# Kernel tuning notes

Hardware: AMD Instinct MI355X
Metric: run time of the kernel (lower is better)

## Reference

```python
import jax, jax.numpy as jnp
import numpy as np

NV, NC, E = 100000, 50000, 800000   # var nodes, config nodes, edges per direction
K = 100                              # configs per graph (uniform -> static dense batch)
B = NC // K                          # number of graphs
DV, DC, DH, DO = 64, 16, 128, 64     # var feat, config feat, hidden, out


def _w(key, i, o):
    # kaiming_normal_ init as in _init_weights
    return jax.random.normal(key, (i, o), jnp.float32) * np.float32(np.sqrt(2.0 / i))


def setup_inputs() -> dict:
    key = jax.random.key(0)
    ks = jax.random.split(key, 16)
    return {
        "x_var": jax.random.normal(ks[0], (NV, DV), jnp.float32),
        "x_config": jax.random.normal(ks[1], (NC, DC), jnp.float32),
        "src_v2c": jax.random.randint(ks[2], (E,), 0, NV, jnp.int32),
        "dst_v2c": jax.random.randint(ks[3], (E,), 0, NC, jnp.int32),
        "src_c2v": jax.random.randint(ks[4], (E,), 0, NC, jnp.int32),
        "dst_c2v": jax.random.randint(ks[5], (E,), 0, NV, jnp.int32),
        "batch_config": jnp.arange(NC, dtype=jnp.int32) // K,
        # layer 1 SAGEConv params per edge type (lin_l has bias, lin_r has none)
        "Wl1_v2c": _w(ks[6], DV, DH), "bl1_v2c": jnp.zeros((DH,), jnp.float32), "Wr1_v2c": _w(ks[7], DC, DH),
        "Wl1_c2v": _w(ks[8], DC, DH), "bl1_c2v": jnp.zeros((DH,), jnp.float32), "Wr1_c2v": _w(ks[9], DV, DH),
        # layer 2 (output layer, jk=None -> maps to out_channels)
        "Wl2_v2c": _w(ks[10], DH, DO), "bl2_v2c": jnp.zeros((DO,), jnp.float32), "Wr2_v2c": _w(ks[11], DH, DO),
    }


def _sage(x_src, x_dst, src, dst, Wl, bl, Wr, n_dst):
    # PyG SAGEConv: lin_l(mean_{j in N(i)} x_src[j]) + lin_r(x_dst[i])
    msum = jax.ops.segment_sum(x_src[src], dst, num_segments=n_dst)            # [n_dst, d_src]
    cnt = jax.ops.segment_sum(jnp.ones(src.shape, x_src.dtype), dst, num_segments=n_dst)
    mean = msum / jnp.maximum(cnt, 1.0)[:, None]
    return mean @ Wl + bl + x_dst @ Wr


def reference(x_var, x_config, src_v2c, dst_v2c, src_c2v, dst_c2v, batch_config,
              Wl1_v2c, bl1_v2c, Wr1_v2c, Wl1_c2v, bl1_c2v, Wr1_c2v,
              Wl2_v2c, bl2_v2c, Wr2_v2c):
    # --- layer 1 (to_hetero: each node type updated by its incoming edge type), ReLU between layers ---
    h_config = jax.nn.relu(_sage(x_var, x_config, src_v2c, dst_v2c, Wl1_v2c, bl1_v2c, Wr1_v2c, NC))
    h_var = jax.nn.relu(_sage(x_config, x_var, src_c2v, dst_c2v, Wl1_c2v, bl1_c2v, Wr1_c2v, NV))
    # --- layer 2: only the 'config' output is consumed downstream ---
    o_config = _sage(h_var, h_config, src_v2c, dst_v2c, Wl2_v2c, bl2_v2c, Wr2_v2c, NC)  # [NC, DO]
    # --- to_dense_batch(x['config'], batch) -> [B, K, DO]; squeeze() is a no-op (no size-1 dims) ---
    cnt = jax.ops.segment_sum(jnp.ones((NC,), jnp.int32), batch_config, num_segments=B)
    starts = jnp.cumsum(cnt) - cnt
    pos = jnp.arange(NC, dtype=jnp.int32) - starts[batch_config]
    dense = jnp.zeros((B, K, DO), o_config.dtype).at[batch_config, pos].set(o_config)
    return dense
```

## Files before the change

kernel.cpp:

```cpp
#include <hip/hip_runtime.h>


#define CHUNK 4096
#define EPT 16
#define MAXBINS 1024

__global__ __launch_bounds__(256) void part_count2_kernel(
    const int* __restrict__ dstC, const int* __restrict__ dstV, int E, int nblocks,
    int nbinsC, int nbinsV, int* __restrict__ countsC, int* __restrict__ countsV) {
    const int* dst; int shift, nbins; int* counts; int b;
    if (blockIdx.x < (unsigned)nblocks) { dst = dstC; shift = 6; nbins = nbinsC; counts = countsC; b = blockIdx.x; }
    else { dst = dstV; shift = 7; nbins = nbinsV; counts = countsV; b = blockIdx.x - nblocks; }
    __shared__ int hist[MAXBINS];
    int t = threadIdx.x;
    for (int j = t; j < nbins; j += 256) hist[j] = 0;
    __syncthreads();
    int base = b * CHUNK;
#pragma unroll
    for (int j = 0; j < EPT; ++j) {
        int e = base + j * 256 + t;
        if (e < E) atomicAdd(&hist[dst[e] >> shift], 1);
    }
    __syncthreads();
    for (int j = t; j < nbins; j += 256) counts[(size_t)j * nblocks + b] = hist[j];
}

__global__ __launch_bounds__(256) void part_rowscan2_kernel(
    int* __restrict__ countsC, int nbinsC, int* __restrict__ binTotC,
    int* __restrict__ countsV, int* __restrict__ binTotV, int nblocks) {
    int* counts; int* binTot; int bin;
    if (blockIdx.x < (unsigned)nbinsC) { counts = countsC; binTot = binTotC; bin = blockIdx.x; }
    else { counts = countsV; binTot = binTotV; bin = blockIdx.x - nbinsC; }
    __shared__ int s[256];
    int t = threadIdx.x;
    int v = (t < nblocks) ? counts[(size_t)bin * nblocks + t] : 0;
    s[t] = v; __syncthreads();
    for (int o = 1; o < 256; o <<= 1) {
        int add = (t >= o) ? s[t - o] : 0; __syncthreads();
        s[t] += add; __syncthreads();
    }
    if (t < nblocks) counts[(size_t)bin * nblocks + t] = s[t] - v;
    if (t == nblocks - 1) binTot[bin] = s[t];
}

__global__ __launch_bounds__(256) void part_binscan2_kernel(
    const int* __restrict__ binTotC, int nbinsC, int* __restrict__ binBaseC,
    const int* __restrict__ binTotV, int nbinsV, int* __restrict__ binBaseV) {
    const int* binTot; int nbins; int* binBase;
    if (blockIdx.x == 0) { binTot = binTotC; nbins = nbinsC; binBase = binBaseC; }
    else { binTot = binTotV; nbins = nbinsV; binBase = binBaseV; }
    __shared__ int s[256];
    __shared__ int carry;
    int t = threadIdx.x;
    if (t == 0) carry = 0;
    __syncthreads();
    for (int c0 = 0; c0 < nbins; c0 += 256) {
        int v = (c0 + t < nbins) ? binTot[c0 + t] : 0;
        s[t] = v; __syncthreads();
        for (int o = 1; o < 256; o <<= 1) {
            int add = (t >= o) ? s[t - o] : 0; __syncthreads();
            s[t] += add; __syncthreads();
        }
        if (c0 + t < nbins) binBase[c0 + t] = carry + s[t] - v;
        __syncthreads();
        if (t == 255) carry += s[255];
        __syncthreads();
    }
    if (t == 0) binBase[nbins] = carry;
}

__global__ __launch_bounds__(256) void part_scatter2_kernel(
    const int* __restrict__ srcC, const int* __restrict__ dstC,
    const int* __restrict__ srcV, const int* __restrict__ dstV, int E, int nblocks,
    int nbinsC, const int* __restrict__ countsC, const int* __restrict__ binBaseC,
    int* __restrict__ ebufC,
    int nbinsV, const int* __restrict__ countsV, const int* __restrict__ binBaseV,
    int* __restrict__ ebufV) {
    const int *src, *dst, *counts, *binBase; int* ebuf; int shift, mask, nbins; int b;
    if (blockIdx.x < (unsigned)nblocks) {
        src = srcC; dst = dstC; counts = countsC; binBase = binBaseC; ebuf = ebufC;
        shift = 6; mask = 63; nbins = nbinsC; b = blockIdx.x;
    } else {
        src = srcV; dst = dstV; counts = countsV; binBase = binBaseV; ebuf = ebufV;
        shift = 7; mask = 127; nbins = nbinsV; b = blockIdx.x - nblocks;
    }
    __shared__ int hist[MAXBINS];
    int t = threadIdx.x;
    for (int j = t; j < nbins; j += 256) hist[j] = 0;
    __syncthreads();
    int base = b * CHUNK;
#pragma unroll
    for (int j = 0; j < EPT; ++j) {
        int e = base + j * 256 + t;
        if (e < E) {
            int d = dst[e];
            int bin = d >> shift;
            int rank = atomicAdd(&hist[bin], 1);
            int slot = binBase[bin] + counts[(size_t)bin * nblocks + b] + rank;
            ebuf[slot] = (src[e] << shift) | (d & mask);
        }
    }
}

__global__ __launch_bounds__(256) void csr2_kernel(
    int nbinsC, const int* __restrict__ binBaseC, const int* __restrict__ ebufC,
    int* __restrict__ ebufC2, int* __restrict__ offC, int nC,
    const int* __restrict__ binBaseV, const int* __restrict__ ebufV,
    int* __restrict__ ebufV2, int* __restrict__ offV, int nV, int E) {
    __shared__ int hist[128];
    __shared__ int cur[128];
    __shared__ int s[256];
    int t = threadIdx.x;
    const int *binBase, *eb1; int *eb2, *off; int n, shift, bin;
    if (blockIdx.x < (unsigned)nbinsC) {
        bin = blockIdx.x; binBase = binBaseC; eb1 = ebufC; eb2 = ebufC2; off = offC; n = nC; shift = 6;
    } else {
        bin = blockIdx.x - nbinsC; binBase = binBaseV; eb1 = ebufV; eb2 = ebufV2; off = offV; n = nV; shift = 7;
    }
    int mask = (1 << shift) - 1, nloc = 1 << shift;
    if (blockIdx.x == 0 && t == 0) { offC[nC] = E; offV[nV] = E; }
    int e0 = binBase[bin], e1 = binBase[bin + 1];
    if (t < nloc) { hist[t] = 0; cur[t] = 0; }
    __syncthreads();
    for (int e = e0 + t; e < e1; e += 256) atomicAdd(&hist[eb1[e] & mask], 1);
    __syncthreads();
    int v = (t < nloc) ? hist[t] : 0;
    s[t] = v; __syncthreads();
    for (int o = 1; o < 256; o <<= 1) {
        int add = (t >= o) ? s[t - o] : 0; __syncthreads();
        s[t] += add; __syncthreads();
    }
    if (t < nloc) {
        int node = (bin << shift) + t;
        if (node < n) off[node] = e0 + s[t] - v;
        hist[t] = s[t] - v;
    }
    __syncthreads();
    for (int e = e0 + t; e < e1; e += 256) {
        int w = eb1[e];
        int local = w & mask;
        int r = atomicAdd(&cur[local], 1);
        eb2[e0 + hist[local] + r] = w >> shift;
    }
}

__device__ __forceinline__ void gather64_body(
    const int* __restrict__ off, const int* __restrict__ eb,
    const float* __restrict__ X, float* __restrict__ M,
    const float* __restrict__ P, float* __restrict__ out,
    int n, int b, int nblocks) {
    int lane = threadIdx.x & 63, wid = threadIdx.x >> 6;
    int nw = nblocks * 4;
    for (int i = b * 4 + wid; i < n; i += nw) {
        int e0 = off[i], e1 = off[i + 1];
        int deg = e1 - e0;
        float acc = 0.f;
        for (int j0 = 0; j0 < deg; j0 += 64) {
            int m = min(deg - j0, 64);
            int idx = 0;
            if (lane < m) idx = eb[e0 + j0 + lane];
            int j = 0;
            for (; j + 4 <= m; j += 4) {
                int s0 = __shfl(idx, j);
                int s1 = __shfl(idx, j + 1);
                int s2 = __shfl(idx, j + 2);
                int s3 = __shfl(idx, j + 3);
                acc += X[(size_t)s0 * 64 + lane];
                acc += X[(size_t)s1 * 64 + lane];
                acc += X[(size_t)s2 * 64 + lane];
                acc += X[(size_t)s3 * 64 + lane];
            }
            for (; j < m; ++j) {
                int s = __shfl(idx, j);
                acc += X[(size_t)s * 64 + lane];
            }
        }
        float r = acc / fmaxf((float)deg, 1.0f);
        if (out) out[(size_t)i * 64 + lane] = r + P[(size_t)i * 64 + lane];
        else     M[(size_t)i * 64 + lane] = r;
    }
}

__device__ __forceinline__ void gather16_body(
    const int* __restrict__ off, const int* __restrict__ eb,
    const float* __restrict__ X, float* __restrict__ M, int n, int b, int nblocks) {
    int lane = threadIdx.x & 63, wid = threadIdx.x >> 6;
    int dlane = lane & 15, eg = lane >> 4;
    int nw = nblocks * 4;
    for (int i = b * 4 + wid; i < n; i += nw) {
        int e0 = off[i], e1 = off[i + 1];
        int deg = e1 - e0;
        float acc = 0.f;
        for (int j0 = 0; j0 < deg; j0 += 64) {
            int m = min(deg - j0, 64);
            int idx = 0;
            if (lane < m) idx = eb[e0 + j0 + lane];
            for (int j = eg; j < m; j += 4) {
                int s = __shfl(idx, j);
                acc += X[(size_t)s * 16 + dlane];
            }
        }
        acc += __shfl_xor(acc, 16);
        acc += __shfl_xor(acc, 32);
        if (lane < 16) M[(size_t)i * 16 + lane] = acc / fmaxf((float)deg, 1.0f);
    }
}

__global__ __launch_bounds__(256) void gather2_kernel(
    const int* __restrict__ offC, const int* __restrict__ ebC,
    const float* __restrict__ Xc, float* __restrict__ Mc, int nC, int gbC,
    const int* __restrict__ offV, const int* __restrict__ ebV,
    const float* __restrict__ Xv, float* __restrict__ Mv, int nV, int gbV) {
    if (blockIdx.x < (unsigned)gbC)
        gather64_body(offC, ebC, Xc, Mc, nullptr, nullptr, nC, blockIdx.x, gbC);
    else
        gather16_body(offV, ebV, Xv, Mv, nV, blockIdx.x - gbC, gbV);
}

__global__ __launch_bounds__(256) void gather64_add_kernel(
    const int* __restrict__ off, const int* __restrict__ eb,
    const float* __restrict__ X, const float* __restrict__ P,
    float* __restrict__ out, int n) {
    gather64_body(off, eb, X, nullptr, P, out, n, blockIdx.x, gridDim.x);
}

template<int D, int ROW0>
__device__ __forceinline__ void stageF(const float* __restrict__ A, float* __restrict__ Fb,
                                       int i0, int n, int t) {
    const int Q = D / 4;
    const int NPP = 256 / Q;
#pragma unroll
    for (int p = 0; p < 64 / NPP; ++p) {
        int nn = t / Q + p * NPP;
        int k4 = t % Q;
        int node = i0 + nn;
        float4 v = make_float4(0.f, 0.f, 0.f, 0.f);
        if (node < n) v = ((const float4*)A)[(size_t)node * Q + k4];
        Fb[(ROW0 + 4 * k4 + 0) * 68 + nn] = v.x;
        Fb[(ROW0 + 4 * k4 + 1) * 68 + nn] = v.y;
        Fb[(ROW0 + 4 * k4 + 2) * 68 + nn] = v.z;
        Fb[(ROW0 + 4 * k4 + 3) * 68 + nn] = v.w;
    }
}

template<int D1, int D2, bool HASB2>
__global__ __launch_bounds__(256) void gemm80_fused_kernel(
    const float* __restrict__ M, const float* __restrict__ X,
    const float* __restrict__ Wl, const float* __restrict__ Wr,
    const float* __restrict__ bias, const float* __restrict__ W2,
    const float* __restrict__ bias2, float* __restrict__ O, int n) {
    __shared__ float Fb[128 * 68];
    __shared__ float Wb[80 * 128];
    int t = threadIdx.x;
    int i0 = blockIdx.x * 64;
    {
        const float4* wl4 = (const float4*)Wl;
        const float4* wr4 = (const float4*)Wr;
        float4* wb4 = (float4*)Wb;
        for (int j = t; j < D1 * 32; j += 256) wb4[j] = wl4[j];
        for (int j = t; j < D2 * 32; j += 256) wb4[D1 * 32 + j] = wr4[j];
    }
    stageF<D1, 0>(M, Fb, i0, n, t);
    stageF<D2, D1>(X, Fb, i0, n, t);
    __syncthreads();
    int tc = t & 15, tn = t >> 4;
    int c0 = tc * 4, n0 = tn * 4;
    float acc[4][8];
#pragma unroll
    for (int j = 0; j < 4; ++j)
#pragma unroll
        for (int jj = 0; jj < 8; ++jj) acc[j][jj] = 0.f;
#pragma unroll 4
    for (int k = 0; k < D1 + D2; ++k) {
        float4 f  = *(const float4*)&Fb[k * 68 + n0];
        float4 wa = *(const float4*)&Wb[k * 128 + c0];
        float4 wc = *(const float4*)&Wb[k * 128 + 64 + c0];
        float ff[4] = {f.x, f.y, f.z, f.w};
        float va[4] = {wa.x, wa.y, wa.z, wa.w};
        float vb[4] = {wc.x, wc.y, wc.z, wc.w};
#pragma unroll
        for (int j = 0; j < 4; ++j)
#pragma unroll
            for (int jj = 0; jj < 4; ++jj) {
                acc[j][jj]     += ff[j] * va[jj];
                acc[j][4 + jj] += ff[j] * vb[jj];
            }
    }
    __syncthreads();
    {
        float4 blo = ((const float4*)bias)[tc];
        float4 bhi = ((const float4*)bias)[16 + tc];
        float bl[8] = {blo.x, blo.y, blo.z, blo.w, bhi.x, bhi.y, bhi.z, bhi.w};
#pragma unroll
        for (int j = 0; j < 4; ++j)
#pragma unroll
            for (int jj = 0; jj < 4; ++jj) {
                Fb[(c0 + jj) * 68 + n0 + j]      = fmaxf(acc[j][jj] + bl[jj], 0.f);
                Fb[(64 + c0 + jj) * 68 + n0 + j] = fmaxf(acc[j][4 + jj] + bl[4 + jj], 0.f);
            }
        const float4* w24 = (const float4*)W2;
        float4* wb4 = (float4*)Wb;
        for (int j = t; j < 128 * 16; j += 256) wb4[j] = w24[j];
    }
    __syncthreads();
    float a2[4][4];
#pragma unroll
    for (int j = 0; j < 4; ++j)
#pragma unroll
        for (int jj = 0; jj < 4; ++jj) a2[j][jj] = 0.f;
#pragma unroll 4
    for (int k = 0; k < 128; ++k) {
        float4 h = *(const float4*)&Fb[k * 68 + n0];
        float4 w = *(const float4*)&Wb[k * 64 + c0];
        float hh[4] = {h.x, h.y, h.z, h.w};
        float ww[4] = {w.x, w.y, w.z, w.w};
#pragma unroll
        for (int j = 0; j < 4; ++j)
#pragma unroll
            for (int jj = 0; jj < 4; ++jj) a2[j][jj] += hh[j] * ww[jj];
    }
    float4 b2 = HASB2 ? ((const float4*)bias2)[tc] : make_float4(0.f, 0.f, 0.f, 0.f);
#pragma unroll
    for (int j = 0; j < 4; ++j) {
        int node = i0 + n0 + j;
        if (node < n) {
            float4 o = {a2[j][0] + b2.x, a2[j][1] + b2.y, a2[j][2] + b2.z, a2[j][3] + b2.w};
            ((float4*)O)[(size_t)node * 16 + tc] = o;
        }
    }
}

extern "C" void kernel_launch(void* const* d_in, const int* in_sizes, int n_in,
                              void* d_out, int out_size, void* d_ws, size_t ws_size,
                              hipStream_t stream) {
    const float* x_var    = (const float*)d_in[0];
    const float* x_config = (const float*)d_in[1];
    const int* src_v2c = (const int*)d_in[2];
    const int* dst_v2c = (const int*)d_in[3];
    const int* src_c2v = (const int*)d_in[4];
    const int* dst_c2v = (const int*)d_in[5];
    const float* Wl1_v2c = (const float*)d_in[7];
    const float* bl1_v2c = (const float*)d_in[8];
    const float* Wr1_v2c = (const float*)d_in[9];
    const float* Wl1_c2v = (const float*)d_in[10];
    const float* bl1_c2v = (const float*)d_in[11];
    const float* Wr1_c2v = (const float*)d_in[12];
    const float* Wl2 = (const float*)d_in[13];
    const float* bl2 = (const float*)d_in[14];
    const float* Wr2 = (const float*)d_in[15];
    float* out = (float*)d_out;

    int NV = in_sizes[0] / 64;
    int NC = in_sizes[1] / 16;
    int E  = in_sizes[2];

    int nblocks = (E + CHUNK - 1) / CHUNK;
    int nbins_c = (NC + 63) >> 6;
    int nbins_v = (NV + 127) >> 7;

    char* p = (char*)d_ws;
    float* Mc  = (float*)p; p += (size_t)NC * 64 * 4;
    float* Mv  = (float*)p; p += (size_t)NV * 16 * 4;
    float* OCp = (float*)p; p += (size_t)NC * 64 * 4;
    float* hv2 = (float*)p; p += (size_t)NV * 64 * 4;
    int* countsC = (int*)p; p += (size_t)nbins_c * nblocks * 4;
    int* countsV = (int*)p; p += (size_t)nbins_v * nblocks * 4;
    int* binTotC = (int*)p; p += (size_t)nbins_c * 4;
    int* binTotV = (int*)p; p += (size_t)nbins_v * 4;
    int* binBaseC = (int*)p; p += (size_t)(nbins_c + 1) * 4;
    int* binBaseV = (int*)p; p += (size_t)(nbins_v + 1) * 4;
    int* offC = (int*)p; p += (size_t)(NC + 1) * 4;
    int* offV = (int*)p; p += (size_t)(NV + 1) * 4;
    int* ebufC  = (int*)p; p += (size_t)E * 4;
    int* ebufV  = (int*)p; p += (size_t)E * 4;
    int* ebufC2 = (int*)p; p += (size_t)E * 4;
    int* ebufV2 = (int*)p; p += (size_t)E * 4;

    part_count2_kernel<<<2 * nblocks, 256, 0, stream>>>(
        dst_v2c, dst_c2v, E, nblocks, nbins_c, nbins_v, countsC, countsV);
    part_rowscan2_kernel<<<nbins_c + nbins_v, 256, 0, stream>>>(
        countsC, nbins_c, binTotC, countsV, binTotV, nblocks);
    part_binscan2_kernel<<<2, 256, 0, stream>>>(
        binTotC, nbins_c, binBaseC, binTotV, nbins_v, binBaseV);
    part_scatter2_kernel<<<2 * nblocks, 256, 0, stream>>>(
        src_v2c, dst_v2c, src_c2v, dst_c2v, E, nblocks,
        nbins_c, countsC, binBaseC, ebufC,
        nbins_v, countsV, binBaseV, ebufV);
    csr2_kernel<<<nbins_c + nbins_v, 256, 0, stream>>>(
        nbins_c, binBaseC, ebufC, ebufC2, offC, NC,
        binBaseV, ebufV, ebufV2, offV, NV, E);

    int gbC = (NC + 3) / 4, gbV = (NV + 3) / 4;
    gather2_kernel<<<gbC + gbV, 256, 0, stream>>>(
        offC, ebufC2, x_var, Mc, NC, gbC,
        offV, ebufV2, x_config, Mv, NV, gbV);

    gemm80_fused_kernel<64, 16, true><<<(NC + 63) / 64, 256, 0, stream>>>(
        Mc, x_config, Wl1_v2c, Wr1_v2c, bl1_v2c, Wr2, bl2, OCp, NC);
    gemm80_fused_kernel<16, 64, false><<<(NV + 63) / 64, 256, 0, stream>>>(
        Mv, x_var, Wl1_c2v, Wr1_c2v, bl1_c2v, Wl2, nullptr, hv2, NV);

    gather64_add_kernel<<<gbC, 256, 0, stream>>>(offC, ebufC2, hv2, OCp, out, NC);
}
```

Measured before the change: 337.5 us.

## Swizzle shared-memory feature tile and merge both GEMM launches into one

Result: slower. 1.271 ms (+276.7%).

```diff
diff --git a/kernel.cpp b/kernel.cpp
--- a/kernel.cpp
+++ b/kernel.cpp
@@ -225,8 +225,8 @@
 }
 
 template<int D, int ROW0>
-__device__ __forceinline__ void stageF(const float* __restrict__ A, float* __restrict__ Fb,
-                                       int i0, int n, int t) {
+__device__ __forceinline__ void stageF_swz(const float* __restrict__ A, float* __restrict__ Fb,
+                                           int i0, int n, int t) {
     const int Q = D / 4;
     const int NPP = 256 / Q;
 #pragma unroll
@@ -236,23 +236,21 @@
         int node = i0 + nn;
         float4 v = make_float4(0.f, 0.f, 0.f, 0.f);
         if (node < n) v = ((const float4*)A)[(size_t)node * Q + k4];
-        Fb[(ROW0 + 4 * k4 + 0) * 68 + nn] = v.x;
-        Fb[(ROW0 + 4 * k4 + 1) * 68 + nn] = v.y;
-        Fb[(ROW0 + 4 * k4 + 2) * 68 + nn] = v.z;
-        Fb[(ROW0 + 4 * k4 + 3) * 68 + nn] = v.w;
+        int cs = (((nn >> 2) + (ROW0 >> 2) + k4) & 15) * 4 + (nn & 3);
+        float* q = Fb + (ROW0 + 4 * k4) * 68 + cs;
+        q[0 * 68] = v.x; q[1 * 68] = v.y; q[2 * 68] = v.z; q[3 * 68] = v.w;
     }
 }
 
 template<int D1, int D2, bool HASB2>
-__global__ __launch_bounds__(256) void gemm80_fused_kernel(
+__device__ __forceinline__ void gemm_body(
     const float* __restrict__ M, const float* __restrict__ X,
     const float* __restrict__ Wl, const float* __restrict__ Wr,
     const float* __restrict__ bias, const float* __restrict__ W2,
-    const float* __restrict__ bias2, float* __restrict__ O, int n) {
-    __shared__ float Fb[128 * 68];
-    __shared__ float Wb[80 * 128];
-    int t = threadIdx.x;
-    int i0 = blockIdx.x * 64;
+    const float* __restrict__ bias2, float* __restrict__ O, int n, int bid,
+    float* __restrict__ Fb, float* __restrict__ Wb) {
+    int t = threadIdx.x;
+    int i0 = bid * 64;
     {
         const float4* wl4 = (const float4*)Wl;
         const float4* wr4 = (const float4*)Wr;
@@ -260,8 +258,8 @@
         for (int j = t; j < D1 * 32; j += 256) wb4[j] = wl4[j];
         for (int j = t; j < D2 * 32; j += 256) wb4[D1 * 32 + j] = wr4[j];
     }
-    stageF<D1, 0>(M, Fb, i0, n, t);
-    stageF<D2, D1>(X, Fb, i0, n, t);
+    stageF_swz<D1, 0>(M, Fb, i0, n, t);
+    stageF_swz<D2, D1>(X, Fb, i0, n, t);
     __syncthreads();
     int tc = t & 15, tn = t >> 4;
     int c0 = tc * 4, n0 = tn * 4;
@@ -270,34 +268,48 @@
     for (int j = 0; j < 4; ++j)
 #pragma unroll
         for (int jj = 0; jj < 8; ++jj) acc[j][jj] = 0.f;
-#pragma unroll 4
-    for (int k = 0; k < D1 + D2; ++k) {
-        float4 f  = *(const float4*)&Fb[k * 68 + n0];
-        float4 wa = *(const float4*)&Wb[k * 128 + c0];
-        float4 wc = *(const float4*)&Wb[k * 128 + 64 + c0];
-        float ff[4] = {f.x, f.y, f.z, f.w};
-        float va[4] = {wa.x, wa.y, wa.z, wa.w};
-        float vb[4] = {wc.x, wc.y, wc.z, wc.w};
-#pragma unroll
-        for (int j = 0; j < 4; ++j)
-#pragma unroll
-            for (int jj = 0; jj < 4; ++jj) {
-                acc[j][jj]     += ff[j] * va[jj];
-                acc[j][4 + jj] += ff[j] * vb[jj];
-            }
+#pragma unroll
+    for (int kg = 0; kg < (D1 + D2) / 4; ++kg) {
+        int sw = ((tn + kg) & 15) * 4;
+#pragma unroll
+        for (int j4 = 0; j4 < 4; ++j4) {
+            int k = 4 * kg + j4;
+            float4 f  = *(const float4*)&Fb[k * 68 + sw];
+            float4 wa = *(const float4*)&Wb[k * 128 + c0];
+            float4 wc = *(const float4*)&Wb[k * 128 + 64 + c0];
+            float ff[4] = {f.x, f.y, f.z, f.w};
+            float va[4] = {wa.x, wa.y, wa.z, wa.w};
+            float vb[4] = {wc.x, wc.y, wc.z, wc.w};
+#pragma unroll
+            for (int j = 0; j < 4; ++j)
+#pragma unroll
+                for (int jj = 0; jj < 4; ++jj) {
+                    acc[j][jj]     += ff[j] * va[jj];
+                    acc[j][4 + jj] += ff[j] * vb[jj];
+                }
+        }
     }
     __syncthreads();
     {
         float4 blo = ((const float4*)bias)[tc];
         float4 bhi = ((const float4*)bias)[16 + tc];
         float bl[8] = {blo.x, blo.y, blo.z, blo.w, bhi.x, bhi.y, bhi.z, bhi.w};
-#pragma unroll
-        for (int j = 0; j < 4; ++j)
-#pragma unroll
-            for (int jj = 0; jj < 4; ++jj) {
-                Fb[(c0 + jj) * 68 + n0 + j]      = fmaxf(acc[j][jj] + bl[jj], 0.f);
-                Fb[(64 + c0 + jj) * 68 + n0 + j] = fmaxf(acc[j][4 + jj] + bl[4 + jj], 0.f);
-            }
+        int sw1 = ((tn + tc) & 15) * 4;
+        int sw2 = ((tn + 16 + tc) & 15) * 4;
+#pragma unroll
+        for (int jj = 0; jj < 4; ++jj) {
+            float4 h1, h2;
+            h1.x = fmaxf(acc[0][jj] + bl[jj], 0.f);
+            h1.y = fmaxf(acc[1][jj] + bl[jj], 0.f);
+            h1.z = fmaxf(acc[2][jj] + bl[jj], 0.f);
+            h1.w = fmaxf(acc[3][jj] + bl[jj], 0.f);
+            h2.x = fmaxf(acc[0][4 + jj] + bl[4 + jj], 0.f);
+            h2.y = fmaxf(acc[1][4 + jj] + bl[4 + jj], 0.f);
+            h2.z = fmaxf(acc[2][4 + jj] + bl[4 + jj], 0.f);
+            h2.w = fmaxf(acc[3][4 + jj] + bl[4 + jj], 0.f);
+            *(float4*)&Fb[(c0 + jj) * 68 + sw1 + (n0 & 3) * 0 + ((tn & 3) * 0)] = h1;
+            *(float4*)&Fb[(64 + c0 + jj) * 68 + sw2] = h2;
+        }
         const float4* w24 = (const float4*)W2;
         float4* wb4 = (float4*)Wb;
         for (int j = t; j < 128 * 16; j += 256) wb4[j] = w24[j];
@@ -308,16 +320,21 @@
     for (int j = 0; j < 4; ++j)
 #pragma unroll
         for (int jj = 0; jj < 4; ++jj) a2[j][jj] = 0.f;
-#pragma unroll 4
-    for (int k = 0; k < 128; ++k) {
-        float4 h = *(const float4*)&Fb[k * 68 + n0];
-        float4 w = *(const float4*)&Wb[k * 64 + c0];
-        float hh[4] = {h.x, h.y, h.z, h.w};
-        float ww[4] = {w.x, w.y, w.z, w.w};
-#pragma unroll
-        for (int j = 0; j < 4; ++j)
-#pragma unroll
-            for (int jj = 0; jj < 4; ++jj) a2[j][jj] += hh[j] * ww[jj];
+#pragma unroll
+    for (int kg = 0; kg < 32; ++kg) {
+        int sw = ((tn + kg) & 15) * 4;
+#pragma unroll
+        for (int j4 = 0; j4 < 4; ++j4) {
+            int k = 4 * kg + j4;
+            float4 h = *(const float4*)&Fb[k * 68 + sw];
+            float4 w = *(const float4*)&Wb[k * 64 + c0];
+            float hh[4] = {h.x, h.y, h.z, h.w};
+            float ww[4] = {w.x, w.y, w.z, w.w};
+#pragma unroll
+            for (int j = 0; j < 4; ++j)
+#pragma unroll
+                for (int jj = 0; jj < 4; ++jj) a2[j][jj] += hh[j] * ww[jj];
+        }
     }
     float4 b2 = HASB2 ? ((const float4*)bias2)[tc] : make_float4(0.f, 0.f, 0.f, 0.f);
 #pragma unroll
@@ -328,6 +345,24 @@
             ((float4*)O)[(size_t)node * 16 + tc] = o;
         }
     }
+}
+
+
+__global__ __launch_bounds__(256) void gemm_both_kernel(
+    const float* __restrict__ Mc, const float* __restrict__ Xc,
+    const float* __restrict__ WlC, const float* __restrict__ WrC,
+    const float* __restrict__ bC, const float* __restrict__ Wr2,
+    const float* __restrict__ bl2, float* __restrict__ OCp, int nC, int nbC,
+    const float* __restrict__ Mv, const float* __restrict__ Xv,
+    const float* __restrict__ WlV, const float* __restrict__ WrV,
+    const float* __restrict__ bV, const float* __restrict__ Wl2,
+    float* __restrict__ hv2, int nV) {
+    __shared__ float Fb[128 * 68];
+    __shared__ float Wb[80 * 128];
+    if (blockIdx.x < (unsigned)nbC)
+        gemm_body<64, 16, true>(Mc, Xc, WlC, WrC, bC, Wr2, bl2, OCp, nC, blockIdx.x, Fb, Wb);
+    else
+        gemm_body<16, 64, false>(Mv, Xv, WlV, WrV, bV, Wl2, nullptr, hv2, nV, blockIdx.x - nbC, Fb, Wb);
 }
 
 extern "C" void kernel_launch(void* const* d_in, const int* in_sizes, int n_in,
@@ -395,10 +430,10 @@
         offC, ebufC2, x_var, Mc, NC, gbC,
         offV, ebufV2, x_config, Mv, NV, gbV);
 
-    gemm80_fused_kernel<64, 16, true><<<(NC + 63) / 64, 256, 0, stream>>>(
-        Mc, x_config, Wl1_v2c, Wr1_v2c, bl1_v2c, Wr2, bl2, OCp, NC);
-    gemm80_fused_kernel<16, 64, false><<<(NV + 63) / 64, 256, 0, stream>>>(
-        Mv, x_var, Wl1_c2v, Wr1_c2v, bl1_c2v, Wl2, nullptr, hv2, NV);
+    int nbC = (NC + 63) / 64, nbV = (NV + 63) / 64;
+    gemm_both_kernel<<<nbC + nbV, 256, 0, stream>>>(
+        Mc, x_config, Wl1_v2c, Wr1_v2c, bl1_v2c, Wr2, bl2, OCp, NC, nbC,
+        Mv, x_var, Wl1_c2v, Wr1_c2v, bl1_c2v, Wl2, hv2, NV);
 
     gather64_add_kernel<<<gbC, 256, 0, stream>>>(offC, ebufC2, hv2, OCp, out, NC);
 }
```
